# Kernel tuning notes

Measured on AMD Instinct MI355X. Metric: run time of the kernel, lower is better.

The kernel has to match this reference:

```python
import jax, jax.numpy as jnp
import numpy as np

GAMMA = 1.4
EPS = 1e-6
N_NEWTON = 20
B, K, NT, NX = 16, 64, 128, 256


def _sound_speed(rho, p):
    return jnp.sqrt(jnp.clip(GAMMA * p / jnp.clip(rho, EPS), EPS))


def setup_inputs() -> dict:
    key = jax.random.key(0)
    k1, k2, k3, k4, k5, k6 = jax.random.split(key, 6)
    xs = jnp.sort(jax.random.uniform(k1, (B, K + 1), dtype=jnp.float32), axis=1)
    ks = jax.random.uniform(k2, (B, K), dtype=jnp.float32, minval=0.1, maxval=1.1)
    ks_v = jax.random.normal(k3, (B, K), dtype=jnp.float32)
    ks_p = jax.random.uniform(k4, (B, K), dtype=jnp.float32, minval=0.1, maxval=1.1)
    pieces_mask = jnp.ones((B, K), dtype=jnp.float32)
    t_coords = jax.random.uniform(k5, (B, NT, NX), dtype=jnp.float32)
    x_coords = jax.random.uniform(k6, (B, NT, NX), dtype=jnp.float32)
    return {"xs": xs, "ks": ks, "ks_v": ks_v, "ks_p": ks_p,
            "pieces_mask": pieces_mask, "t_coords": t_coords, "x_coords": x_coords}


def reference(xs, ks, ks_v, ks_p, pieces_mask, t_coords, x_coords):
    gm1 = GAMMA - 1.0
    gp1 = GAMMA + 1.0
    exp_rare = gm1 / (2.0 * GAMMA)

    # left/right states at the K-1 interfaces: (B, K-1)
    rho_L, rho_R = ks[:, :-1], ks[:, 1:]
    u_L, u_R = ks_v[:, :-1], ks_v[:, 1:]
    p_L, p_R = ks_p[:, :-1], ks_p[:, 1:]

    c_L = _sound_speed(rho_L, p_L)
    c_R = _sound_speed(rho_R, p_R)
    A_L = 2.0 / (gp1 * jnp.clip(rho_L, EPS))
    A_R = 2.0 / (gp1 * jnp.clip(rho_R, EPS))
    B_L = gm1 / gp1 * p_L
    B_R = gm1 / gp1 * p_R

    def wave_f_df(p, p_K, A_K, B_K, c_K):
        denom = jnp.clip(p + B_K, EPS)
        sqrt_AoD = jnp.sqrt(jnp.clip(A_K / denom, EPS))
        f_shock = (p - p_K) * sqrt_AoD
        df_shock = sqrt_AoD * (1.0 - (p - p_K) / (2.0 * denom))
        p_ratio = jnp.clip(p / jnp.clip(p_K, EPS), EPS)
        f_rare = 2.0 * c_K / gm1 * (p_ratio ** exp_rare - 1.0)
        df_rare = c_K / (GAMMA * jnp.clip(p_K, EPS)) * p_ratio ** (-gp1 / (2.0 * GAMMA))
        is_shock = p > p_K
        return jnp.where(is_shock, f_shock, f_rare), jnp.where(is_shock, df_shock, df_rare)

    # two-rarefaction initial guess
    p0 = jnp.clip(((c_L + c_R - gm1 / 2.0 * (u_R - u_L)) /
                   (c_L / jnp.clip(p_L, EPS) ** exp_rare +
                    c_R / jnp.clip(p_R, EPS) ** exp_rare)) ** (1.0 / exp_rare), EPS)

    def newton_step(i, p_star):
        f_L, df_L = wave_f_df(p_star, p_L, A_L, B_L, c_L)
        f_R, df_R = wave_f_df(p_star, p_R, A_R, B_R, c_R)
        residual = f_L + f_R + (u_R - u_L)
        jacobian = jnp.clip(df_L + df_R, EPS)
        return jnp.clip(p_star - residual / jacobian, EPS)

    p_star = jax.lax.fori_loop(0, N_NEWTON, newton_step, p0)

    f_L, _ = wave_f_df(p_star, p_L, A_L, B_L, c_L)
    f_R, _ = wave_f_df(p_star, p_R, A_R, B_R, c_R)
    u_star = 0.5 * (u_L + u_R) + 0.5 * (f_R - f_L)  # computed as in source (unused downstream)

    gp1_o_2g = gp1 / (2.0 * GAMMA)
    sigma_1 = u_L - c_L * jnp.sqrt(jnp.clip(1.0 + gp1_o_2g * (p_star / jnp.clip(p_L, EPS) - 1.0), EPS))
    speed_left = jnp.where(p_star > p_L, sigma_1, u_L - c_L)
    sigma_3 = u_R + c_R * jnp.sqrt(jnp.clip(1.0 + gp1_o_2g * (p_star / jnp.clip(p_R, EPS) - 1.0), EPS))
    speed_right = jnp.where(p_star > p_R, sigma_3, u_R + c_R)

    x_d = xs[:, 1:K][:, None, None, :]           # (B,1,1,K-1)
    sr = speed_right[:, None, None, :]
    sl = speed_left[:, None, None, :]
    xi = (x_coords[..., None] - x_d) / (t_coords[..., None] + EPS)  # (B,nt,nx,K-1)

    penalty_left_seg = jax.nn.relu(xi - sr)
    penalty_right_seg = jax.nn.relu(sl - xi)
    pad_last = ((0, 0), (0, 0), (0, 0), (0, 1))
    pad_first = ((0, 0), (0, 0), (0, 0), (1, 0))
    bias = -(jnp.pad(penalty_left_seg, pad_last) + jnp.pad(penalty_right_seg, pad_first))

    mask = pieces_mask[:, None, None, :]
    bias = bias * mask + (mask == 0).astype(bias.dtype) * (-1e9)
    return bias
```

## Files before the change

### kernel.cpp

```cpp
#include <hip/hip_runtime.h>
#include <math.h>

#define GAMMA_F 1.4f
#define EPS_F 1e-6f
#define B_ 16
#define K_ 64
#define NT_ 128
#define NX_ 256
#define NI 63
#define N_NEWTON 20

#define PTS_PER_ITER 16
#define ITERS 8
#define PTS_PER_BLOCK (PTS_PER_ITER * ITERS)
#define BLOCKS_PER_B (NT_ * NX_ / PTS_PER_BLOCK)

typedef float floatx4 __attribute__((ext_vector_type(4)));

__device__ __forceinline__ void wave_f_df(float p, float p_K, float A_K, float B_K,
                                          float c_K, float& f, float& df) {
    const float gm1 = GAMMA_F - 1.0f;
    const float exp_rare = gm1 / (2.0f * GAMMA_F);
    float denom = fmaxf(p + B_K, EPS_F);
    float sqrt_AoD = sqrtf(fmaxf(A_K / denom, EPS_F));
    float f_shock = (p - p_K) * sqrt_AoD;
    float df_shock = sqrt_AoD * (1.0f - (p - p_K) / (2.0f * denom));
    float pKc = fmaxf(p_K, EPS_F);
    float p_ratio = fmaxf(p / pKc, EPS_F);
    float pre = powf(p_ratio, exp_rare);
    float f_rare = 2.0f * c_K / gm1 * (pre - 1.0f);
    float df_rare = c_K / (GAMMA_F * pKc) * (pre / p_ratio);
    bool is_shock = p > p_K;
    f = is_shock ? f_shock : f_rare;
    df = is_shock ? df_shock : df_rare;
}

__global__ void riemann_solve_kernel(const float* __restrict__ xs,
                                     const float* __restrict__ ks,
                                     const float* __restrict__ ks_v,
                                     const float* __restrict__ ks_p,
                                     float* __restrict__ sr_ws,
                                     float* __restrict__ sl_ws,
                                     float* __restrict__ xd_ws) {
    const int b = blockIdx.x;
    const int i = threadIdx.x;
    if (i >= NI) return;

    const float gm1 = GAMMA_F - 1.0f;
    const float gp1 = GAMMA_F + 1.0f;
    const float exp_rare = gm1 / (2.0f * GAMMA_F);

    const int base = b * K_ + i;
    float rho_L = ks[base],     rho_R = ks[base + 1];
    float u_L   = ks_v[base],   u_R   = ks_v[base + 1];
    float p_L   = ks_p[base],   p_R   = ks_p[base + 1];
    const float du = u_R - u_L;

    float c_L = sqrtf(fmaxf(GAMMA_F * p_L / fmaxf(rho_L, EPS_F), EPS_F));
    float c_R = sqrtf(fmaxf(GAMMA_F * p_R / fmaxf(rho_R, EPS_F), EPS_F));
    float A_L = 2.0f / (gp1 * fmaxf(rho_L, EPS_F));
    float A_R = 2.0f / (gp1 * fmaxf(rho_R, EPS_F));
    float B_L = gm1 / gp1 * p_L;
    float B_R = gm1 / gp1 * p_R;

    float num = c_L + c_R - 0.5f * gm1 * du;
    float den = c_L / powf(fmaxf(p_L, EPS_F), exp_rare)
              + c_R / powf(fmaxf(p_R, EPS_F), exp_rare);
    float p_star = fmaxf(powf(num / den, 1.0f / exp_rare), EPS_F);

    #pragma unroll 1
    for (int it = 0; it < N_NEWTON; ++it) {
        float fL, dfL, fR, dfR;
        wave_f_df(p_star, p_L, A_L, B_L, c_L, fL, dfL);
        wave_f_df(p_star, p_R, A_R, B_R, c_R, fR, dfR);
        float residual = fL + fR + du;
        float jac = fmaxf(dfL + dfR, EPS_F);
        p_star = fmaxf(p_star - residual / jac, EPS_F);
    }

    const float gp1_o_2g = gp1 / (2.0f * GAMMA_F);
    float s1 = u_L - c_L * sqrtf(fmaxf(1.0f + gp1_o_2g * (p_star / fmaxf(p_L, EPS_F) - 1.0f), EPS_F));
    float speed_left = (p_star > p_L) ? s1 : (u_L - c_L);
    float s3 = u_R + c_R * sqrtf(fmaxf(1.0f + gp1_o_2g * (p_star / fmaxf(p_R, EPS_F) - 1.0f), EPS_F));
    float speed_right = (p_star > p_R) ? s3 : (u_R + c_R);

    sl_ws[base] = speed_left;
    sr_ws[base] = speed_right;
    xd_ws[base] = xs[b * (K_ + 1) + i + 1];
}

__global__ __launch_bounds__(256) void
bias_kernel(const float* __restrict__ t_coords,
            const float* __restrict__ x_coords,
            const float* __restrict__ pieces_mask,
            const float* __restrict__ sr_ws,
            const float* __restrict__ sl_ws,
            const float* __restrict__ xd_ws,
            float* __restrict__ out) {
    __shared__ float s_sr[NI];
    __shared__ float s_sl[NI];
    __shared__ float s_xd[NI];
    __shared__ float s_mask[K_];

    const int bid = blockIdx.x;
    const int b = bid >> 8;
    const int blk_in_b = bid & 255;
    const int tid = threadIdx.x;

    {
        const int g = tid >> 6;
        const int r = tid & 63;
        if (g == 0) { if (r < NI) s_sr[r] = sr_ws[b * K_ + r]; }
        else if (g == 1) { if (r < NI) s_sl[r] = sl_ws[b * K_ + r]; }
        else if (g == 2) { if (r < NI) s_xd[r] = xd_ws[b * K_ + r]; }
        else { s_mask[r] = pieces_mask[b * K_ + r]; }
    }
    __syncthreads();

    const int p_local = tid >> 4;
    const int j = tid & 15;
    const int k0 = j << 2;

    float xdr[5];
    #pragma unroll
    for (int q = -1; q <= 3; ++q) {
        int k = k0 + q;
        xdr[q + 1] = (k >= 0 && k < NI) ? s_xd[k] : 0.0f;
    }
    float srr[4], slr[4], mkr[4], madd[4];
    #pragma unroll
    for (int q = 0; q < 4; ++q) {
        int k = k0 + q;
        srr[q] = (k < NI) ? s_sr[k] : 3.0e38f;
        slr[q] = (k >= 1) ? s_sl[k - 1] : -3.0e38f;
        float m = s_mask[k];
        mkr[q] = m;
        madd[q] = (m == 0.0f) ? -1.0e9f : 0.0f;
    }

    const int pt0 = blk_in_b * PTS_PER_BLOCK + p_local;
    const long long bbase = (long long)b * (NT_ * NX_);
    const float* tp = t_coords + bbase + pt0;
    const float* xp = x_coords + bbase + pt0;
    float* op = out + (bbase + pt0) * (long long)K_ + k0;

    #pragma unroll
    for (int it = 0; it < ITERS; ++it) {
        const float t = tp[it * PTS_PER_ITER];
        const float x = xp[it * PTS_PER_ITER];
        const float inv_t = 1.0f / (t + EPS_F);

        float xi[5];
        #pragma unroll
        for (int q = 0; q < 5; ++q)
            xi[q] = (x - xdr[q]) * inv_t;

        float r0, r1, r2, r3;
        {
            float pl, pr;
            pl = fmaxf(xi[1] - srr[0], 0.0f);
            pr = fmaxf(slr[0] - xi[0], 0.0f);
            r0 = -(pl + pr) * mkr[0] + madd[0];
            pl = fmaxf(xi[2] - srr[1], 0.0f);
            pr = fmaxf(slr[1] - xi[1], 0.0f);
            r1 = -(pl + pr) * mkr[1] + madd[1];
            pl = fmaxf(xi[3] - srr[2], 0.0f);
            pr = fmaxf(slr[2] - xi[2], 0.0f);
            r2 = -(pl + pr) * mkr[2] + madd[2];
            pl = fmaxf(xi[4] - srr[3], 0.0f);
            pr = fmaxf(slr[3] - xi[3], 0.0f);
            r3 = -(pl + pr) * mkr[3] + madd[3];
        }

        floatx4 v;
        v.x = r0; v.y = r1; v.z = r2; v.w = r3;
        __builtin_nontemporal_store(v, reinterpret_cast<floatx4*>(op));
        op += PTS_PER_ITER * K_;
    }
}

extern "C" void kernel_launch(void* const* d_in, const int* in_sizes, int n_in,
                              void* d_out, int out_size, void* d_ws, size_t ws_size,
                              hipStream_t stream) {
    const float* xs          = (const float*)d_in[0];
    const float* ks          = (const float*)d_in[1];
    const float* ks_v        = (const float*)d_in[2];
    const float* ks_p        = (const float*)d_in[3];
    const float* pieces_mask = (const float*)d_in[4];
    const float* t_coords    = (const float*)d_in[5];
    const float* x_coords    = (const float*)d_in[6];
    float* out = (float*)d_out;

    float* ws = (float*)d_ws;
    float* sr_ws = ws;
    float* sl_ws = ws + B_ * K_;
    float* xd_ws = ws + 2 * B_ * K_;

    riemann_solve_kernel<<<B_, 64, 0, stream>>>(xs, ks, ks_v, ks_p, sr_ws, sl_ws, xd_ws);

    const int blocks = B_ * BLOCKS_PER_B;
    bias_kernel<<<blocks, 256, 0, stream>>>(t_coords, x_coords, pieces_mask,
                                            sr_ws, sl_ws, xd_ws, out);
}
```

Measured before the change: 176.4 us.

## Fuse Riemann solve into bias kernel and double points per block

Removes the separate Riemann-solver launch and its workspace round trip. Each bias block now recomputes the 63 interface solves (20 Newton iterations with powf) for its batch in one wavefront, writing the speeds straight to shared memory. ITERS is doubled so there are half as many blocks, which spreads the redundant solve over more output points. The trade-off is that every block repeats the serial Newton loop before its store phase, which may add latency to a kernel that is bound by output bandwidth.

```diff
diff --git a/kernel.cpp b/kernel.cpp
--- a/kernel.cpp
+++ b/kernel.cpp
@@ -11,7 +11,7 @@
 #define N_NEWTON 20
 
 #define PTS_PER_ITER 16
-#define ITERS 8
+#define ITERS 16
 #define PTS_PER_BLOCK (PTS_PER_ITER * ITERS)
 #define BLOCKS_PER_B (NT_ * NX_ / PTS_PER_BLOCK)
 
@@ -35,85 +35,71 @@
     df = is_shock ? df_shock : df_rare;
 }
 
-__global__ void riemann_solve_kernel(const float* __restrict__ xs,
-                                     const float* __restrict__ ks,
-                                     const float* __restrict__ ks_v,
-                                     const float* __restrict__ ks_p,
-                                     float* __restrict__ sr_ws,
-                                     float* __restrict__ sl_ws,
-                                     float* __restrict__ xd_ws) {
-    const int b = blockIdx.x;
-    const int i = threadIdx.x;
-    if (i >= NI) return;
-
-    const float gm1 = GAMMA_F - 1.0f;
-    const float gp1 = GAMMA_F + 1.0f;
-    const float exp_rare = gm1 / (2.0f * GAMMA_F);
-
-    const int base = b * K_ + i;
-    float rho_L = ks[base],     rho_R = ks[base + 1];
-    float u_L   = ks_v[base],   u_R   = ks_v[base + 1];
-    float p_L   = ks_p[base],   p_R   = ks_p[base + 1];
-    const float du = u_R - u_L;
-
-    float c_L = sqrtf(fmaxf(GAMMA_F * p_L / fmaxf(rho_L, EPS_F), EPS_F));
-    float c_R = sqrtf(fmaxf(GAMMA_F * p_R / fmaxf(rho_R, EPS_F), EPS_F));
-    float A_L = 2.0f / (gp1 * fmaxf(rho_L, EPS_F));
-    float A_R = 2.0f / (gp1 * fmaxf(rho_R, EPS_F));
-    float B_L = gm1 / gp1 * p_L;
-    float B_R = gm1 / gp1 * p_R;
-
-    float num = c_L + c_R - 0.5f * gm1 * du;
-    float den = c_L / powf(fmaxf(p_L, EPS_F), exp_rare)
-              + c_R / powf(fmaxf(p_R, EPS_F), exp_rare);
-    float p_star = fmaxf(powf(num / den, 1.0f / exp_rare), EPS_F);
-
-    #pragma unroll 1
-    for (int it = 0; it < N_NEWTON; ++it) {
-        float fL, dfL, fR, dfR;
-        wave_f_df(p_star, p_L, A_L, B_L, c_L, fL, dfL);
-        wave_f_df(p_star, p_R, A_R, B_R, c_R, fR, dfR);
-        float residual = fL + fR + du;
-        float jac = fmaxf(dfL + dfR, EPS_F);
-        p_star = fmaxf(p_star - residual / jac, EPS_F);
-    }
-
-    const float gp1_o_2g = gp1 / (2.0f * GAMMA_F);
-    float s1 = u_L - c_L * sqrtf(fmaxf(1.0f + gp1_o_2g * (p_star / fmaxf(p_L, EPS_F) - 1.0f), EPS_F));
-    float speed_left = (p_star > p_L) ? s1 : (u_L - c_L);
-    float s3 = u_R + c_R * sqrtf(fmaxf(1.0f + gp1_o_2g * (p_star / fmaxf(p_R, EPS_F) - 1.0f), EPS_F));
-    float speed_right = (p_star > p_R) ? s3 : (u_R + c_R);
-
-    sl_ws[base] = speed_left;
-    sr_ws[base] = speed_right;
-    xd_ws[base] = xs[b * (K_ + 1) + i + 1];
-}
-
 __global__ __launch_bounds__(256) void
-bias_kernel(const float* __restrict__ t_coords,
-            const float* __restrict__ x_coords,
-            const float* __restrict__ pieces_mask,
-            const float* __restrict__ sr_ws,
-            const float* __restrict__ sl_ws,
-            const float* __restrict__ xd_ws,
-            float* __restrict__ out) {
+fused_bias_kernel(const float* __restrict__ xs,
+                  const float* __restrict__ ks,
+                  const float* __restrict__ ks_v,
+                  const float* __restrict__ ks_p,
+                  const float* __restrict__ pieces_mask,
+                  const float* __restrict__ t_coords,
+                  const float* __restrict__ x_coords,
+                  float* __restrict__ out) {
     __shared__ float s_sr[NI];
     __shared__ float s_sl[NI];
     __shared__ float s_xd[NI];
     __shared__ float s_mask[K_];
 
     const int bid = blockIdx.x;
-    const int b = bid >> 8;
-    const int blk_in_b = bid & 255;
+    const int b = bid >> 7;
+    const int blk_in_b = bid & 127;
     const int tid = threadIdx.x;
 
-    {
-        const int g = tid >> 6;
-        const int r = tid & 63;
-        if (g == 0) { if (r < NI) s_sr[r] = sr_ws[b * K_ + r]; }
-        else if (g == 1) { if (r < NI) s_sl[r] = sl_ws[b * K_ + r]; }
-        else if (g == 2) { if (r < NI) s_xd[r] = xd_ws[b * K_ + r]; }
-        else { s_mask[r] = pieces_mask[b * K_ + r]; }
+    if (tid < NI) {
+        const int i = tid;
+        const float gm1 = GAMMA_F - 1.0f;
+        const float gp1 = GAMMA_F + 1.0f;
+        const float exp_rare = gm1 / (2.0f * GAMMA_F);
+
+        const int base = b * K_ + i;
+        float rho_L = ks[base],     rho_R = ks[base + 1];
+        float u_L   = ks_v[base],   u_R   = ks_v[base + 1];
+        float p_L   = ks_p[base],   p_R   = ks_p[base + 1];
+        const float du = u_R - u_L;
+
+        float c_L = sqrtf(fmaxf(GAMMA_F * p_L / fmaxf(rho_L, EPS_F), EPS_F));
+        float c_R = sqrtf(fmaxf(GAMMA_F * p_R / fmaxf(rho_R, EPS_F), EPS_F));
+        float A_L = 2.0f / (gp1 * fmaxf(rho_L, EPS_F));
+        float A_R = 2.0f / (gp1 * fmaxf(rho_R, EPS_F));
+        float B_L = gm1 / gp1 * p_L;
+        float B_R = gm1 / gp1 * p_R;
+
+        float num = c_L + c_R - 0.5f * gm1 * du;
+        float den = c_L / powf(fmaxf(p_L, EPS_F), exp_rare)
+                  + c_R / powf(fmaxf(p_R, EPS_F), exp_rare);
+        float p_star = fmaxf(powf(num / den, 1.0f / exp_rare), EPS_F);
+
+        #pragma unroll 1
+        for (int it = 0; it < N_NEWTON; ++it) {
+            float fL, dfL, fR, dfR;
+            wave_f_df(p_star, p_L, A_L, B_L, c_L, fL, dfL);
+            wave_f_df(p_star, p_R, A_R, B_R, c_R, fR, dfR);
+            float residual = fL + fR + du;
+            float jac = fmaxf(dfL + dfR, EPS_F);
+            p_star = fmaxf(p_star - residual / jac, EPS_F);
+        }
+
+        const float gp1_o_2g = gp1 / (2.0f * GAMMA_F);
+        float s1 = u_L - c_L * sqrtf(fmaxf(1.0f + gp1_o_2g * (p_star / fmaxf(p_L, EPS_F) - 1.0f), EPS_F));
+        float speed_left = (p_star > p_L) ? s1 : (u_L - c_L);
+        float s3 = u_R + c_R * sqrtf(fmaxf(1.0f + gp1_o_2g * (p_star / fmaxf(p_R, EPS_F) - 1.0f), EPS_F));
+        float speed_right = (p_star > p_R) ? s3 : (u_R + c_R);
+
+        s_sl[i] = speed_left;
+        s_sr[i] = speed_right;
+        s_xd[i] = xs[b * (K_ + 1) + i + 1];
+    } else if (tid >= 64 && tid < 64 + K_) {
+        const int r = tid - 64;
+        s_mask[r] = pieces_mask[b * K_ + r];
     }
     __syncthreads();
 
@@ -191,14 +177,7 @@
     const float* x_coords    = (const float*)d_in[6];
     float* out = (float*)d_out;
 
-    float* ws = (float*)d_ws;
-    float* sr_ws = ws;
-    float* sl_ws = ws + B_ * K_;
-    float* xd_ws = ws + 2 * B_ * K_;
-
-    riemann_solve_kernel<<<B_, 64, 0, stream>>>(xs, ks, ks_v, ks_p, sr_ws, sl_ws, xd_ws);
-
     const int blocks = B_ * BLOCKS_PER_B;
-    bias_kernel<<<blocks, 256, 0, stream>>>(t_coords, x_coords, pieces_mask,
-                                            sr_ws, sl_ws, xd_ws, out);
+    fused_bias_kernel<<<blocks, 256, 0, stream>>>(xs, ks, ks_v, ks_p, pieces_mask,
+                                                  t_coords, x_coords, out);
 }
```

New measurement: 183.4 us. +4.0%, slower.
